# Kernel tuning notes

Hardware: AMD Instinct MI355X
Metric: run time of the kernel (lower is better)

## Reference

```python
import jax, jax.numpy as jnp
import numpy as np

N_NODES = 50000
N_EDGES = 800000
IN_DIM = 128
HID = 64
HEADS = 2
OUT_DIM = 2
N_GRAPHS = 512
NEG_SLOPE = 0.2


def setup_inputs() -> dict:
    key = jax.random.key(0)
    ks = jax.random.split(key, 16)
    x = jax.random.normal(ks[0], (N_NODES, IN_DIM), dtype=jnp.float32)
    edge_index = jax.random.randint(ks[1], (2, N_EDGES), 0, N_NODES, dtype=jnp.int64)
    batch = jnp.sort(jax.random.randint(ks[2], (N_NODES,), 0, N_GRAPHS, dtype=jnp.int64))
    s = 0.1
    W1 = jax.random.normal(ks[3], (IN_DIM, HEADS * HID), dtype=jnp.float32) * s
    a_src1 = jax.random.normal(ks[4], (HEADS, HID), dtype=jnp.float32) * s
    a_dst1 = jax.random.normal(ks[5], (HEADS, HID), dtype=jnp.float32) * s
    b1 = jnp.zeros((HEADS * HID,), dtype=jnp.float32)
    W2 = jax.random.normal(ks[6], (HEADS * HID, HID), dtype=jnp.float32) * s
    a_src2 = jax.random.normal(ks[7], (1, HID), dtype=jnp.float32) * s
    a_dst2 = jax.random.normal(ks[8], (1, HID), dtype=jnp.float32) * s
    b2 = jnp.zeros((HID,), dtype=jnp.float32)
    fcW = jax.random.normal(ks[9], (HID, OUT_DIM), dtype=jnp.float32) * s
    fcb = jnp.zeros((OUT_DIM,), dtype=jnp.float32)
    return dict(x=x, edge_index=edge_index, batch=batch,
                W1=W1, a_src1=a_src1, a_dst1=a_dst1, b1=b1,
                W2=W2, a_src2=a_src2, a_dst2=a_dst2, b2=b2,
                fcW=fcW, fcb=fcb)


def gat_layer(x, src, dst, W, a_src, a_dst, b, heads, c_out):
    # x: [N, F] -> h: [N, H, C]
    N = x.shape[0]
    h = (x @ W).reshape(N, heads, c_out)
    alpha_s = jnp.sum(h * a_src, axis=-1)  # [N, H]
    alpha_d = jnp.sum(h * a_dst, axis=-1)  # [N, H]
    e = jax.nn.leaky_relu(alpha_s[src] + alpha_d[dst], NEG_SLOPE)  # [E, H]
    # segment softmax over destination nodes
    emax = jax.ops.segment_max(e, dst, num_segments=N)  # [N, H]
    ex = jnp.exp(e - emax[dst])
    denom = jax.ops.segment_sum(ex, dst, num_segments=N)  # [N, H]
    coef = ex / denom[dst]  # [E, H]
    msg = h[src] * coef[..., None]  # [E, H, C]
    out = jax.ops.segment_sum(msg, dst, num_segments=N)  # [N, H, C]
    return out.reshape(N, heads * c_out) + b


def reference(x, edge_index, batch, W1, a_src1, a_dst1, b1, W2, a_src2, a_dst2, b2, fcW, fcb):
    N = x.shape[0]
    # PyG GATConv add_self_loops=True (shared graph for both layers)
    loops = jnp.arange(N, dtype=edge_index.dtype)
    src = jnp.concatenate([edge_index[0], loops])
    dst = jnp.concatenate([edge_index[1], loops])
    h = jax.nn.relu(gat_layer(x, src, dst, W1, a_src1, a_dst1, b1, HEADS, HID))
    h = jax.nn.relu(gat_layer(h, src, dst, W2, a_src2, a_dst2, b2, 1, HID))
    # global mean pool over graphs
    sums = jax.ops.segment_sum(h, batch, num_segments=N_GRAPHS)  # [G, HID]
    cnts = jax.ops.segment_sum(jnp.ones((N,), dtype=h.dtype), batch, num_segments=N_GRAPHS)
    pooled = sums / jnp.maximum(cnts, 1.0)[:, None]
    logits = pooled @ fcW + fcb
    return jax.nn.log_softmax(logits, axis=1)
```

## Files before the change

kernel.cpp:

```cpp
#include <hip/hip_runtime.h>
#include <math.h>

#define N_NODES 50000
#define N_EDGES 800000
#define EP (N_EDGES + N_NODES)
#define IN_DIM 128
#define HID 64
#define HEADS 2
#define OUT_DIM 2
#define N_GRAPHS 512
#define NEG_SLOPE 0.2f
#define NB_SCAN 196

typedef unsigned int uint;
typedef unsigned short ushort;

__device__ __forceinline__ ushort f2bf(float f) {
    uint u = __float_as_uint(f);
    u += 0x7fffu + ((u >> 16) & 1u);
    return (ushort)(u >> 16);
}
__device__ __forceinline__ float bf_lo(uint u) { return __uint_as_float(u << 16); }
__device__ __forceinline__ float bf_hi(uint u) { return __uint_as_float(u & 0xffff0000u); }

__global__ void hist_kernel(const int* __restrict__ ei, int* __restrict__ cnt,
                            int* __restrict__ erank) {
    int i = blockIdx.x * blockDim.x + threadIdx.x;
    if (i >= EP) return;
    int d = (i < N_EDGES) ? ei[N_EDGES + i] : (i - N_EDGES);
    erank[i] = atomicAdd(&cnt[d], 1);
}

__global__ void partial_kernel(const int* __restrict__ cnt, int* __restrict__ bsum) {
    int tid = threadIdx.x;
    int i = blockIdx.x * 256 + tid;
    int lane = tid & 63, wid = tid >> 6;
    int v = (i < N_NODES) ? cnt[i] : 0;
#pragma unroll
    for (int off = 32; off; off >>= 1) v += __shfl_xor(v, off);
    __shared__ int wsum[4];
    if (lane == 0) wsum[wid] = v;
    __syncthreads();
    if (tid == 0) bsum[blockIdx.x] = wsum[0] + wsum[1] + wsum[2] + wsum[3];
}

__global__ void scanb_kernel(const int* __restrict__ bsum, int* __restrict__ boff,
                             int* __restrict__ rowptr) {
    int tid = threadIdx.x;
    int lane = tid & 63, wid = tid >> 6;
    int v = (tid < NB_SCAN) ? bsum[tid] : 0;
    int incl = v;
#pragma unroll
    for (int off = 1; off < 64; off <<= 1) {
        int t = __shfl_up(incl, off);
        if (lane >= off) incl += t;
    }
    __shared__ int wt[4];
    if (lane == 63) wt[wid] = incl;
    __syncthreads();
    int add = 0;
    for (int w = 0; w < wid; w++) add += wt[w];
    incl += add;
    if (tid < NB_SCAN) boff[tid] = incl - v;
    if (tid == NB_SCAN - 1) rowptr[N_NODES] = incl;
}

__global__ void scanc_kernel(const int* __restrict__ cnt, const int* __restrict__ boff,
                             int* __restrict__ rowptr) {
    int tid = threadIdx.x;
    int i = blockIdx.x * 256 + tid;
    int lane = tid & 63, wid = tid >> 6;
    int v = (i < N_NODES) ? cnt[i] : 0;
    int incl = v;
#pragma unroll
    for (int off = 1; off < 64; off <<= 1) {
        int t = __shfl_up(incl, off);
        if (lane >= off) incl += t;
    }
    __shared__ int wt[4];
    if (lane == 63) wt[wid] = incl;
    __syncthreads();
    int add = boff[blockIdx.x];
    for (int w = 0; w < wid; w++) add += wt[w];
    int excl = add + incl - v;
    if (i < N_NODES) rowptr[i] = excl;
}

__global__ void scatter_kernel(const int* __restrict__ ei, const int* __restrict__ rowptr,
                               const int* __restrict__ erank, int* __restrict__ csr_src) {
    int i = blockIdx.x * blockDim.x + threadIdx.x;
    if (i >= EP) return;
    int s, d;
    if (i < N_EDGES) { s = ei[i]; d = ei[N_EDGES + i]; }
    else             { s = d = i - N_EDGES; }
    csr_src[rowptr[d] + erank[i]] = s;
}

__global__ void gemm_alphas1(const float* __restrict__ X, const float* __restrict__ W,
                             ushort* __restrict__ Y,
                             const float* __restrict__ a_src, const float* __restrict__ a_dst,
                             float* __restrict__ as, float* __restrict__ ad, int n_nodes) {
    __shared__ float xs[8][128];
    const int base = blockIdx.x * 8;
    const int t = threadIdx.x;
    const float4* X4 = (const float4*)X;
    for (int idx = t; idx < 8 * 32; idx += 64) {
        int r = idx >> 5, c = idx & 31;
        int n = base + r;
        float4 v = (n < n_nodes) ? X4[(size_t)n * 32 + c] : make_float4(0.f, 0.f, 0.f, 0.f);
        ((float4*)xs[r])[c] = v;
    }
    __syncthreads();

    float acc0[8], acc1[8];
#pragma unroll
    for (int i = 0; i < 8; i++) { acc0[i] = 0.f; acc1[i] = 0.f; }
    for (int k = 0; k < 128; k += 4) {
        float wA[4], wB[4];
#pragma unroll
        for (int kk = 0; kk < 4; kk++) {
            wA[kk] = W[(size_t)(k + kk) * 128 + t];
            wB[kk] = W[(size_t)(k + kk) * 128 + 64 + t];
        }
#pragma unroll
        for (int i = 0; i < 8; i++) {
            float4 xv = *(const float4*)&xs[i][k];
            float xx0 = xv.x, xx1 = xv.y, xx2 = xv.z, xx3 = xv.w;
            acc0[i] = fmaf(xx0, wA[0], acc0[i]); acc1[i] = fmaf(xx0, wB[0], acc1[i]);
            acc0[i] = fmaf(xx1, wA[1], acc0[i]); acc1[i] = fmaf(xx1, wB[1], acc1[i]);
            acc0[i] = fmaf(xx2, wA[2], acc0[i]); acc1[i] = fmaf(xx2, wB[2], acc1[i]);
            acc0[i] = fmaf(xx3, wA[3], acc0[i]); acc1[i] = fmaf(xx3, wB[3], acc1[i]);
        }
    }

    const float asv0 = a_src[t],      adv0 = a_dst[t];
    const float asv1 = a_src[64 + t], adv1 = a_dst[64 + t];
#pragma unroll
    for (int i = 0; i < 8; i++) {
        int n = base + i;
        if (n >= n_nodes) continue;
        Y[(size_t)n * 128 + t]      = f2bf(acc0[i]);
        Y[(size_t)n * 128 + 64 + t] = f2bf(acc1[i]);
        float s0 = acc0[i] * asv0, d0 = acc0[i] * adv0;
        float s1 = acc1[i] * asv1, d1 = acc1[i] * adv1;
#pragma unroll
        for (int off = 32; off; off >>= 1) {
            s0 += __shfl_xor(s0, off);
            d0 += __shfl_xor(d0, off);
            s1 += __shfl_xor(s1, off);
            d1 += __shfl_xor(d1, off);
        }
        if (t == 0) {
            as[(size_t)n * 2 + 0] = s0; as[(size_t)n * 2 + 1] = s1;
            ad[(size_t)n * 2 + 0] = d0; ad[(size_t)n * 2 + 1] = d1;
        }
    }
}

__global__ void gemm_alphas2(const float* __restrict__ X, const float* __restrict__ W,
                             ushort* __restrict__ Y,
                             const float* __restrict__ a_src, const float* __restrict__ a_dst,
                             float* __restrict__ as, float* __restrict__ ad, int n_nodes) {
    __shared__ float xs[8][128];
    const int base = blockIdx.x * 8;
    const int t = threadIdx.x;
    const int g = t >> 5, c = t & 31;
    const float4* X4 = (const float4*)X;
    for (int idx = t; idx < 8 * 32; idx += 64) {
        int r = idx >> 5, cc = idx & 31;
        int n = base + r;
        float4 v = (n < n_nodes) ? X4[(size_t)n * 32 + cc] : make_float4(0.f, 0.f, 0.f, 0.f);
        ((float4*)xs[r])[cc] = v;
    }
    __syncthreads();

    float acc0[4], acc1[4];
#pragma unroll
    for (int i = 0; i < 4; i++) { acc0[i] = 0.f; acc1[i] = 0.f; }
    for (int k = 0; k < 128; k += 4) {
        float wA[4], wB[4];
#pragma unroll
        for (int kk = 0; kk < 4; kk++) {
            wA[kk] = W[(size_t)(k + kk) * 64 + c];
            wB[kk] = W[(size_t)(k + kk) * 64 + 32 + c];
        }
#pragma unroll
        for (int i = 0; i < 4; i++) {
            float4 xv = *(const float4*)&xs[g * 4 + i][k];
            float xx0 = xv.x, xx1 = xv.y, xx2 = xv.z, xx3 = xv.w;
            acc0[i] = fmaf(xx0, wA[0], acc0[i]); acc1[i] = fmaf(xx0, wB[0], acc1[i]);
            acc0[i] = fmaf(xx1, wA[1], acc0[i]); acc1[i] = fmaf(xx1, wB[1], acc1[i]);
            acc0[i] = fmaf(xx2, wA[2], acc0[i]); acc1[i] = fmaf(xx2, wB[2], acc1[i]);
            acc0[i] = fmaf(xx3, wA[3], acc0[i]); acc1[i] = fmaf(xx3, wB[3], acc1[i]);
        }
    }

    const float asvA = a_src[c], asvB = a_src[32 + c];
    const float advA = a_dst[c], advB = a_dst[32 + c];
#pragma unroll
    for (int i = 0; i < 4; i++) {
        int n = base + g * 4 + i;
        if (n >= n_nodes) continue;
        Y[(size_t)n * 64 + c]      = f2bf(acc0[i]);
        Y[(size_t)n * 64 + 32 + c] = f2bf(acc1[i]);
        float s = acc0[i] * asvA + acc1[i] * asvB;
        float d = acc0[i] * advA + acc1[i] * advB;
#pragma unroll
        for (int off = 16; off; off >>= 1) {
            s += __shfl_xor(s, off);
            d += __shfl_xor(d, off);
        }
        if (c == 0) { as[n] = s; ad[n] = d; }
    }
}

__device__ __forceinline__ float lrelu(float e) { return e > 0.f ? e : NEG_SLOPE * e; }

__global__ void node_agg1_kernel(const int* __restrict__ rowptr, const int* __restrict__ csr_src,
                                 const uint* __restrict__ Hb,
                                 const float* __restrict__ as, const float* __restrict__ ad,
                                 const float* __restrict__ b, float* __restrict__ outp) {
    int wave = threadIdx.x >> 6;
    int lane = threadIdx.x & 63;
    int node = blockIdx.x * 4 + wave;
    if (node >= N_NODES) return;
    const int lo = rowptr[node], hi = rowptr[node + 1];
    const float ad0 = ad[(size_t)node * 2 + 0], ad1 = ad[(size_t)node * 2 + 1];

    float exa0 = 0.f, exa1 = 0.f, exb0 = 0.f, exb1 = 0.f;
    int j1 = lo + lane;
    if (j1 < hi) {
        int s = csr_src[j1];
        float2 a = *(const float2*)&as[(size_t)s * 2];
        exa0 = __expf(lrelu(a.x + ad0));
        exa1 = __expf(lrelu(a.y + ad1));
    }
    int j2 = lo + 64 + lane;
    if (j2 < hi) {
        int s = csr_src[j2];
        float2 a = *(const float2*)&as[(size_t)s * 2];
        exb0 = __expf(lrelu(a.x + ad0));
        exb1 = __expf(lrelu(a.y + ad1));
    }
    float d0 = exa0 + exb0, d1 = exa1 + exb1;
    for (int j = lo + 128 + lane; j < hi; j += 64) {
        int s = csr_src[j];
        float2 a = *(const float2*)&as[(size_t)s * 2];
        d0 += __expf(lrelu(a.x + ad0));
        d1 += __expf(lrelu(a.y + ad1));
    }
#pragma unroll
    for (int off = 32; off; off >>= 1) {
        d0 += __shfl_xor(d0, off);
        d1 += __shfl_xor(d1, off);
    }
    const float inv = (lane < 32) ? (1.f / d0) : (1.f / d1);
    const bool h0side = (lane < 32);

    float acc0 = 0.f, acc1 = 0.f;
    const int deg = hi - lo;
    const int n1 = deg < 64 ? deg : 64;
    int j = 0;
    for (; j + 4 <= n1; j += 4) {
        int s0 = csr_src[lo + j + 0], s1 = csr_src[lo + j + 1];
        int s2 = csr_src[lo + j + 2], s3 = csr_src[lo + j + 3];
        float ca0 = __shfl(exa0, j + 0), cb0 = __shfl(exa1, j + 0);
        float ca1 = __shfl(exa0, j + 1), cb1 = __shfl(exa1, j + 1);
        float ca2 = __shfl(exa0, j + 2), cb2 = __shfl(exa1, j + 2);
        float ca3 = __shfl(exa0, j + 3), cb3 = __shfl(exa1, j + 3);
        float c0 = h0side ? ca0 : cb0;
        float c1 = h0side ? ca1 : cb1;
        float c2 = h0side ? ca2 : cb2;
        float c3 = h0side ? ca3 : cb3;
        uint u0 = Hb[(size_t)s0 * 64 + lane];
        uint u1 = Hb[(size_t)s1 * 64 + lane];
        uint u2 = Hb[(size_t)s2 * 64 + lane];
        uint u3 = Hb[(size_t)s3 * 64 + lane];
        acc0 = fmaf(bf_lo(u0), c0, acc0); acc1 = fmaf(bf_hi(u0), c0, acc1);
        acc0 = fmaf(bf_lo(u1), c1, acc0); acc1 = fmaf(bf_hi(u1), c1, acc1);
        acc0 = fmaf(bf_lo(u2), c2, acc0); acc1 = fmaf(bf_hi(u2), c2, acc1);
        acc0 = fmaf(bf_lo(u3), c3, acc0); acc1 = fmaf(bf_hi(u3), c3, acc1);
    }
    for (; j < n1; j++) {
        int s = csr_src[lo + j];
        float ca = __shfl(exa0, j), cb = __shfl(exa1, j);
        float c = h0side ? ca : cb;
        uint u = Hb[(size_t)s * 64 + lane];
        acc0 = fmaf(bf_lo(u), c, acc0);
        acc1 = fmaf(bf_hi(u), c, acc1);
    }
    if (deg > 64) {
        const int n2 = deg < 128 ? deg : 128;
        for (j = 64; j < n2; j++) {
            int s = csr_src[lo + j];
            float ca = __shfl(exb0, j - 64), cb = __shfl(exb1, j - 64);
            float c = h0side ? ca : cb;
            uint u = Hb[(size_t)s * 64 + lane];
            acc0 = fmaf(bf_lo(u), c, acc0);
            acc1 = fmaf(bf_hi(u), c, acc1);
        }
        for (int jj = lo + 128; jj < hi; jj++) {
            int s = csr_src[jj];
            float2 a = *(const float2*)&as[(size_t)s * 2];
            float e0 = __expf(lrelu(a.x + ad0));
            float e1 = __expf(lrelu(a.y + ad1));
            float c = h0side ? e0 : e1;
            uint u = Hb[(size_t)s * 64 + lane];
            acc0 = fmaf(bf_lo(u), c, acc0);
            acc1 = fmaf(bf_hi(u), c, acc1);
        }
    }
    float v0 = acc0 * inv + b[2 * lane];
    float v1 = acc1 * inv + b[2 * lane + 1];
    v0 = v0 > 0.f ? v0 : 0.f;
    v1 = v1 > 0.f ? v1 : 0.f;
    *(float2*)&outp[(size_t)node * 128 + 2 * lane] = make_float2(v0, v1);
}

__global__ void node_agg2_kernel(const int* __restrict__ rowptr, const int* __restrict__ csr_src,
                                 const ushort* __restrict__ Hb,
                                 const float* __restrict__ as, const float* __restrict__ ad,
                                 const float* __restrict__ b, float* __restrict__ outp) {
    int wave = threadIdx.x >> 6;
    int lane = threadIdx.x & 63;
    int node = blockIdx.x * 4 + wave;
    if (node >= N_NODES) return;
    const int lo = rowptr[node], hi = rowptr[node + 1];
    const float adN = ad[node];

    float exa = 0.f, exb = 0.f;
    int j1 = lo + lane;
    if (j1 < hi) exa = __expf(lrelu(as[csr_src[j1]] + adN));
    int j2 = lo + 64 + lane;
    if (j2 < hi) exb = __expf(lrelu(as[csr_src[j2]] + adN));
    float d = exa + exb;
    for (int j = lo + 128 + lane; j < hi; j += 64)
        d += __expf(lrelu(as[csr_src[j]] + adN));
#pragma unroll
    for (int off = 32; off; off >>= 1) d += __shfl_xor(d, off);
    const float inv = 1.f / d;

    float acc = 0.f;
    const int deg = hi - lo;
    const int n1 = deg < 64 ? deg : 64;
    int j = 0;
    for (; j + 4 <= n1; j += 4) {
        int s0 = csr_src[lo + j + 0], s1 = csr_src[lo + j + 1];
        int s2 = csr_src[lo + j + 2], s3 = csr_src[lo + j + 3];
        float c0 = __shfl(exa, j + 0), c1 = __shfl(exa, j + 1);
        float c2 = __shfl(exa, j + 2), c3 = __shfl(exa, j + 3);
        float h0 = __uint_as_float(((uint)Hb[(size_t)s0 * 64 + lane]) << 16);
        float h1 = __uint_as_float(((uint)Hb[(size_t)s1 * 64 + lane]) << 16);
        float h2 = __uint_as_float(((uint)Hb[(size_t)s2 * 64 + lane]) << 16);
        float h3 = __uint_as_float(((uint)Hb[(size_t)s3 * 64 + lane]) << 16);
        acc = fmaf(h0, c0, acc);
        acc = fmaf(h1, c1, acc);
        acc = fmaf(h2, c2, acc);
        acc = fmaf(h3, c3, acc);
    }
    for (; j < n1; j++) {
        float c = __shfl(exa, j);
        acc = fmaf(__uint_as_float(((uint)Hb[(size_t)csr_src[lo + j] * 64 + lane]) << 16), c, acc);
    }
    if (deg > 64) {
        const int n2 = deg < 128 ? deg : 128;
        for (j = 64; j < n2; j++) {
            float c = __shfl(exb, j - 64);
            acc = fmaf(__uint_as_float(((uint)Hb[(size_t)csr_src[lo + j] * 64 + lane]) << 16), c, acc);
        }
        for (int jj = lo + 128; jj < hi; jj++) {
            int s = csr_src[jj];
            float c = __expf(lrelu(as[s] + adN));
            acc = fmaf(__uint_as_float(((uint)Hb[(size_t)s * 64 + lane]) << 16), c, acc);
        }
    }
    float v = acc * inv + b[lane];
    outp[(size_t)node * 64 + lane] = v > 0.f ? v : 0.f;
}

__global__ void pool_fc_kernel(const float* __restrict__ act2,
                               const int* __restrict__ batch,
                               const float* __restrict__ fcW,
                               const float* __restrict__ fcb,
                               float* __restrict__ out) {
    int g = blockIdx.x;
    int tid = threadIdx.x;
    int wid = tid >> 6, c = tid & 63;
    __shared__ int slo, shi;
    if (tid == 0) {
        int lo = 0, hi = N_NODES;
        while (lo < hi) { int m = (lo + hi) >> 1; if (batch[m] < g) lo = m + 1; else hi = m; }
        slo = lo;
        lo = 0; hi = N_NODES;
        while (lo < hi) { int m = (lo + hi) >> 1; if (batch[m] < g + 1) lo = m + 1; else hi = m; }
        shi = lo;
    }
    __syncthreads();
    const int lo = slo, hi = shi;
    float sum = 0.f;
    for (int n = lo + wid; n < hi; n += 4) sum += act2[(size_t)n * HID + c];
    __shared__ float ps[4][HID];
    ps[wid][c] = sum;
    __syncthreads();
    if (wid == 0) {
        float t = ps[0][c] + ps[1][c] + ps[2][c] + ps[3][c];
        float cnt = (float)(hi - lo);
        __shared__ float pooled[HID];
        pooled[c] = t / fmaxf(cnt, 1.f);
        __syncthreads();
        __shared__ float ls[OUT_DIM];
        if (c < OUT_DIM) {
            float l = fcb[c];
#pragma unroll 8
            for (int k = 0; k < HID; k++) l = fmaf(pooled[k], fcW[k * OUT_DIM + c], l);
            ls[c] = l;
        }
        __syncthreads();
        if (c < OUT_DIM) {
            float m = fmaxf(ls[0], ls[1]);
            float lse = m + logf(expf(ls[0] - m) + expf(ls[1] - m));
            out[(size_t)g * OUT_DIM + c] = ls[c] - lse;
        }
    }
}

extern "C" void kernel_launch(void* const* d_in, const int* in_sizes, int n_in,
                              void* d_out, int out_size, void* d_ws, size_t ws_size,
                              hipStream_t stream) {
    const float* x    = (const float*)d_in[0];
    const int*   ei   = (const int*)d_in[1];
    const int*   batch= (const int*)d_in[2];
    const float* W1   = (const float*)d_in[3];
    const float* as1w = (const float*)d_in[4];
    const float* ad1w = (const float*)d_in[5];
    const float* b1   = (const float*)d_in[6];
    const float* W2   = (const float*)d_in[7];
    const float* as2w = (const float*)d_in[8];
    const float* ad2w = (const float*)d_in[9];
    const float* b2   = (const float*)d_in[10];
    const float* fcW  = (const float*)d_in[11];
    const float* fcb  = (const float*)d_in[12];

    const size_t N = N_NODES;
    float* ws = (float*)d_ws;
    ushort* h1b  = (ushort*)ws;
    float* act1  = ws + N * 64;
    ushort* h2b  = (ushort*)(act1 + N * 128);
    float* out2  = act1 + N * 128 + N * 32;
    float* alps1 = out2 + N * 64;
    float* alpd1 = alps1 + N * 2;
    float* alps2 = alpd1 + N * 2;
    float* alpd2 = alps2 + N;
    int* cnt     = (int*)(alpd2 + N);
    int* rowptr  = cnt + N;
    int* bsum    = rowptr + N + 1;
    int* boff    = bsum + NB_SCAN;
    int* erank   = boff + NB_SCAN;
    int* csr_src = erank + EP;

    hipMemsetAsync(cnt, 0, N * sizeof(int), stream);
    hist_kernel<<<(EP + 255) / 256, 256, 0, stream>>>(ei, cnt, erank);
    partial_kernel<<<NB_SCAN, 256, 0, stream>>>(cnt, bsum);
    scanb_kernel<<<1, 256, 0, stream>>>(bsum, boff, rowptr);
    scanc_kernel<<<NB_SCAN, 256, 0, stream>>>(cnt, boff, rowptr);
    scatter_kernel<<<(EP + 255) / 256, 256, 0, stream>>>(ei, rowptr, erank, csr_src);

    gemm_alphas1<<<(N + 7) / 8, 64, 0, stream>>>(
        x, W1, h1b, as1w, ad1w, alps1, alpd1, (int)N);
    node_agg1_kernel<<<(N + 3) / 4, 256, 0, stream>>>(
        rowptr, csr_src, (const uint*)h1b, alps1, alpd1, b1, act1);

    gemm_alphas2<<<(N + 7) / 8, 64, 0, stream>>>(
        act1, W2, h2b, as2w, ad2w, alps2, alpd2, (int)N);
    node_agg2_kernel<<<(N + 3) / 4, 256, 0, stream>>>(
        rowptr, csr_src, h2b, alps2, alpd2, b2, out2);

    pool_fc_kernel<<<N_GRAPHS, 256, 0, stream>>>(out2, batch, fcW, fcb, (float*)d_out);
}
```

Before: 310.5 us.

## Fuse layer-1 GEMM with edge histogram and widen aggregation unroll to 8

Merges the layer-1 projection GEMM and the destination-degree histogram into one launch. Blocks are partitioned by index: the first group does the GEMM with 4 waves per block, each wave owning 8 nodes, and the rest do the atomic histogram. This lets the independent compute-bound and atomic-bound work overlap and removes one launch. Both aggregation kernels also unroll the neighbor loop from 4 to 8 and issue all gathers before the shuffles, for more memory-level parallelism at the cost of extra registers.

```diff
diff --git a/kernel.cpp b/kernel.cpp
--- a/kernel.cpp
+++ b/kernel.cpp
@@ -11,6 +11,8 @@
 #define N_GRAPHS 512
 #define NEG_SLOPE 0.2f
 #define NB_SCAN 196
+#define G_GEMM1 1563
+#define G_HIST 3321
 
 typedef unsigned int uint;
 typedef unsigned short ushort;
@@ -23,12 +25,75 @@
 __device__ __forceinline__ float bf_lo(uint u) { return __uint_as_float(u << 16); }
 __device__ __forceinline__ float bf_hi(uint u) { return __uint_as_float(u & 0xffff0000u); }
 
-__global__ void hist_kernel(const int* __restrict__ ei, int* __restrict__ cnt,
-                            int* __restrict__ erank) {
-    int i = blockIdx.x * blockDim.x + threadIdx.x;
-    if (i >= EP) return;
-    int d = (i < N_EDGES) ? ei[N_EDGES + i] : (i - N_EDGES);
-    erank[i] = atomicAdd(&cnt[d], 1);
+__global__ void fused_gemm1_hist(const float* __restrict__ X, const float* __restrict__ W,
+                                 ushort* __restrict__ Y,
+                                 const float* __restrict__ a_src, const float* __restrict__ a_dst,
+                                 float* __restrict__ as, float* __restrict__ ad,
+                                 const int* __restrict__ ei, int* __restrict__ cnt,
+                                 int* __restrict__ erank) {
+    if (blockIdx.x >= G_GEMM1) {
+        int i = (blockIdx.x - G_GEMM1) * 256 + threadIdx.x;
+        if (i < EP) {
+            int d = (i < N_EDGES) ? ei[N_EDGES + i] : (i - N_EDGES);
+            erank[i] = atomicAdd(&cnt[d], 1);
+        }
+        return;
+    }
+    __shared__ float xs[32][128];
+    const int wave = threadIdx.x >> 6;
+    const int lane = threadIdx.x & 63;
+    const int base = blockIdx.x * 32 + wave * 8;
+    const float4* X4 = (const float4*)X;
+    for (int idx = lane; idx < 8 * 32; idx += 64) {
+        int r = idx >> 5, c = idx & 31;
+        int n = base + r;
+        float4 v = (n < N_NODES) ? X4[(size_t)n * 32 + c] : make_float4(0.f, 0.f, 0.f, 0.f);
+        ((float4*)xs[wave * 8 + r])[c] = v;
+    }
+    __syncthreads();
+
+    float acc0[8], acc1[8];
+#pragma unroll
+    for (int i = 0; i < 8; i++) { acc0[i] = 0.f; acc1[i] = 0.f; }
+    for (int k = 0; k < 128; k += 4) {
+        float wA[4], wB[4];
+#pragma unroll
+        for (int kk = 0; kk < 4; kk++) {
+            wA[kk] = W[(size_t)(k + kk) * 128 + lane];
+            wB[kk] = W[(size_t)(k + kk) * 128 + 64 + lane];
+        }
+#pragma unroll
+        for (int i = 0; i < 8; i++) {
+            float4 xv = *(const float4*)&xs[wave * 8 + i][k];
+            acc0[i] = fmaf(xv.x, wA[0], acc0[i]); acc1[i] = fmaf(xv.x, wB[0], acc1[i]);
+            acc0[i] = fmaf(xv.y, wA[1], acc0[i]); acc1[i] = fmaf(xv.y, wB[1], acc1[i]);
+            acc0[i] = fmaf(xv.z, wA[2], acc0[i]); acc1[i] = fmaf(xv.z, wB[2], acc1[i]);
+            acc0[i] = fmaf(xv.w, wA[3], acc0[i]); acc1[i] = fmaf(xv.w, wB[3], acc1[i]);
+        }
+    }
+
+    const float asv0 = a_src[lane],      adv0 = a_dst[lane];
+    const float asv1 = a_src[64 + lane], adv1 = a_dst[64 + lane];
+#pragma unroll
+    for (int i = 0; i < 8; i++) {
+        int n = base + i;
+        if (n >= N_NODES) continue;
+        Y[(size_t)n * 128 + lane]      = f2bf(acc0[i]);
+        Y[(size_t)n * 128 + 64 + lane] = f2bf(acc1[i]);
+        float s0 = acc0[i] * asv0, d0 = acc0[i] * adv0;
+        float s1 = acc1[i] * asv1, d1 = acc1[i] * adv1;
+#pragma unroll
+        for (int off = 32; off; off >>= 1) {
+            s0 += __shfl_xor(s0, off);
+            d0 += __shfl_xor(d0, off);
+            s1 += __shfl_xor(s1, off);
+            d1 += __shfl_xor(d1, off);
+        }
+        if (lane == 0) {
+            as[(size_t)n * 2 + 0] = s0; as[(size_t)n * 2 + 1] = s1;
+            ad[(size_t)n * 2 + 0] = d0; ad[(size_t)n * 2 + 1] = d1;
+        }
+    }
 }
 
 __global__ void partial_kernel(const int* __restrict__ cnt, int* __restrict__ bsum) {
@@ -94,67 +159,6 @@
     if (i < N_EDGES) { s = ei[i]; d = ei[N_EDGES + i]; }
     else             { s = d = i - N_EDGES; }
     csr_src[rowptr[d] + erank[i]] = s;
-}
-
-__global__ void gemm_alphas1(const float* __restrict__ X, const float* __restrict__ W,
-                             ushort* __restrict__ Y,
-                             const float* __restrict__ a_src, const float* __restrict__ a_dst,
-                             float* __restrict__ as, float* __restrict__ ad, int n_nodes) {
-    __shared__ float xs[8][128];
-    const int base = blockIdx.x * 8;
-    const int t = threadIdx.x;
-    const float4* X4 = (const float4*)X;
-    for (int idx = t; idx < 8 * 32; idx += 64) {
-        int r = idx >> 5, c = idx & 31;
-        int n = base + r;
-        float4 v = (n < n_nodes) ? X4[(size_t)n * 32 + c] : make_float4(0.f, 0.f, 0.f, 0.f);
-        ((float4*)xs[r])[c] = v;
-    }
-    __syncthreads();
-
-    float acc0[8], acc1[8];
-#pragma unroll
-    for (int i = 0; i < 8; i++) { acc0[i] = 0.f; acc1[i] = 0.f; }
-    for (int k = 0; k < 128; k += 4) {
-        float wA[4], wB[4];
-#pragma unroll
-        for (int kk = 0; kk < 4; kk++) {
-            wA[kk] = W[(size_t)(k + kk) * 128 + t];
-            wB[kk] = W[(size_t)(k + kk) * 128 + 64 + t];
-        }
-#pragma unroll
-        for (int i = 0; i < 8; i++) {
-            float4 xv = *(const float4*)&xs[i][k];
-            float xx0 = xv.x, xx1 = xv.y, xx2 = xv.z, xx3 = xv.w;
-            acc0[i] = fmaf(xx0, wA[0], acc0[i]); acc1[i] = fmaf(xx0, wB[0], acc1[i]);
-            acc0[i] = fmaf(xx1, wA[1], acc0[i]); acc1[i] = fmaf(xx1, wB[1], acc1[i]);
-            acc0[i] = fmaf(xx2, wA[2], acc0[i]); acc1[i] = fmaf(xx2, wB[2], acc1[i]);
-            acc0[i] = fmaf(xx3, wA[3], acc0[i]); acc1[i] = fmaf(xx3, wB[3], acc1[i]);
-        }
-    }
-
-    const float asv0 = a_src[t],      adv0 = a_dst[t];
-    const float asv1 = a_src[64 + t], adv1 = a_dst[64 + t];
-#pragma unroll
-    for (int i = 0; i < 8; i++) {
-        int n = base + i;
-        if (n >= n_nodes) continue;
-        Y[(size_t)n * 128 + t]      = f2bf(acc0[i]);
-        Y[(size_t)n * 128 + 64 + t] = f2bf(acc1[i]);
-        float s0 = acc0[i] * asv0, d0 = acc0[i] * adv0;
-        float s1 = acc1[i] * asv1, d1 = acc1[i] * adv1;
-#pragma unroll
-        for (int off = 32; off; off >>= 1) {
-            s0 += __shfl_xor(s0, off);
-            d0 += __shfl_xor(d0, off);
-            s1 += __shfl_xor(s1, off);
-            d1 += __shfl_xor(d1, off);
-        }
-        if (t == 0) {
-            as[(size_t)n * 2 + 0] = s0; as[(size_t)n * 2 + 1] = s1;
-            ad[(size_t)n * 2 + 0] = d0; ad[(size_t)n * 2 + 1] = d1;
-        }
-    }
 }
 
 __global__ void gemm_alphas2(const float* __restrict__ X, const float* __restrict__ W,
@@ -187,11 +191,10 @@
 #pragma unroll
         for (int i = 0; i < 4; i++) {
             float4 xv = *(const float4*)&xs[g * 4 + i][k];
-            float xx0 = xv.x, xx1 = xv.y, xx2 = xv.z, xx3 = xv.w;
-            acc0[i] = fmaf(xx0, wA[0], acc0[i]); acc1[i] = fmaf(xx0, wB[0], acc1[i]);
-            acc0[i] = fmaf(xx1, wA[1], acc0[i]); acc1[i] = fmaf(xx1, wB[1], acc1[i]);
-            acc0[i] = fmaf(xx2, wA[2], acc0[i]); acc1[i] = fmaf(xx2, wB[2], acc1[i]);
-            acc0[i] = fmaf(xx3, wA[3], acc0[i]); acc1[i] = fmaf(xx3, wB[3], acc1[i]);
+            acc0[i] = fmaf(xv.x, wA[0], acc0[i]); acc1[i] = fmaf(xv.x, wB[0], acc1[i]);
+            acc0[i] = fmaf(xv.y, wA[1], acc0[i]); acc1[i] = fmaf(xv.y, wB[1], acc1[i]);
+            acc0[i] = fmaf(xv.z, wA[2], acc0[i]); acc1[i] = fmaf(xv.z, wB[2], acc1[i]);
+            acc0[i] = fmaf(xv.w, wA[3], acc0[i]); acc1[i] = fmaf(xv.w, wB[3], acc1[i]);
         }
     }
 
@@ -261,25 +264,43 @@
     const int deg = hi - lo;
     const int n1 = deg < 64 ? deg : 64;
     int j = 0;
-    for (; j + 4 <= n1; j += 4) {
+    for (; j + 8 <= n1; j += 8) {
         int s0 = csr_src[lo + j + 0], s1 = csr_src[lo + j + 1];
         int s2 = csr_src[lo + j + 2], s3 = csr_src[lo + j + 3];
+        int s4 = csr_src[lo + j + 4], s5 = csr_src[lo + j + 5];
+        int s6 = csr_src[lo + j + 6], s7 = csr_src[lo + j + 7];
+        uint u0 = Hb[(size_t)s0 * 64 + lane];
+        uint u1 = Hb[(size_t)s1 * 64 + lane];
+        uint u2 = Hb[(size_t)s2 * 64 + lane];
+        uint u3 = Hb[(size_t)s3 * 64 + lane];
+        uint u4 = Hb[(size_t)s4 * 64 + lane];
+        uint u5 = Hb[(size_t)s5 * 64 + lane];
+        uint u6 = Hb[(size_t)s6 * 64 + lane];
+        uint u7 = Hb[(size_t)s7 * 64 + lane];
         float ca0 = __shfl(exa0, j + 0), cb0 = __shfl(exa1, j + 0);
         float ca1 = __shfl(exa0, j + 1), cb1 = __shfl(exa1, j + 1);
         float ca2 = __shfl(exa0, j + 2), cb2 = __shfl(exa1, j + 2);
         float ca3 = __shfl(exa0, j + 3), cb3 = __shfl(exa1, j + 3);
+        float ca4 = __shfl(exa0, j + 4), cb4 = __shfl(exa1, j + 4);
+        float ca5 = __shfl(exa0, j + 5), cb5 = __shfl(exa1, j + 5);
+        float ca6 = __shfl(exa0, j + 6), cb6 = __shfl(exa1, j + 6);
+        float ca7 = __shfl(exa0, j + 7), cb7 = __shfl(exa1, j + 7);
         float c0 = h0side ? ca0 : cb0;
         float c1 = h0side ? ca1 : cb1;
         float c2 = h0side ? ca2 : cb2;
         float c3 = h0side ? ca3 : cb3;
-        uint u0 = Hb[(size_t)s0 * 64 + lane];
-        uint u1 = Hb[(size_t)s1 * 64 + lane];
-        uint u2 = Hb[(size_t)s2 * 64 + lane];
-        uint u3 = Hb[(size_t)s3 * 64 + lane];
+        float c4 = h0side ? ca4 : cb4;
+        float c5 = h0side ? ca5 : cb5;
+        float c6 = h0side ? ca6 : cb6;
+        float c7 = h0side ? ca7 : cb7;
         acc0 = fmaf(bf_lo(u0), c0, acc0); acc1 = fmaf(bf_hi(u0), c0, acc1);
         acc0 = fmaf(bf_lo(u1), c1, acc0); acc1 = fmaf(bf_hi(u1), c1, acc1);
         acc0 = fmaf(bf_lo(u2), c2, acc0); acc1 = fmaf(bf_hi(u2), c2, acc1);
         acc0 = fmaf(bf_lo(u3), c3, acc0); acc1 = fmaf(bf_hi(u3), c3, acc1);
+        acc0 = fmaf(bf_lo(u4), c4, acc0); acc1 = fmaf(bf_hi(u4), c4, acc1);
+        acc0 = fmaf(bf_lo(u5), c5, acc0); acc1 = fmaf(bf_hi(u5), c5, acc1);
+        acc0 = fmaf(bf_lo(u6), c6, acc0); acc1 = fmaf(bf_hi(u6), c6, acc1);
+        acc0 = fmaf(bf_lo(u7), c7, acc0); acc1 = fmaf(bf_hi(u7), c7, acc1);
     }
     for (; j < n1; j++) {
         int s = csr_src[lo + j];
@@ -344,19 +365,31 @@
     const int deg = hi - lo;
     const int n1 = deg < 64 ? deg : 64;
     int j = 0;
-    for (; j + 4 <= n1; j += 4) {
+    for (; j + 8 <= n1; j += 8) {
         int s0 = csr_src[lo + j + 0], s1 = csr_src[lo + j + 1];
         int s2 = csr_src[lo + j + 2], s3 = csr_src[lo + j + 3];
-        float c0 = __shfl(exa, j + 0), c1 = __shfl(exa, j + 1);
-        float c2 = __shfl(exa, j + 2), c3 = __shfl(exa, j + 3);
+        int s4 = csr_src[lo + j + 4], s5 = csr_src[lo + j + 5];
+        int s6 = csr_src[lo + j + 6], s7 = csr_src[lo + j + 7];
         float h0 = __uint_as_float(((uint)Hb[(size_t)s0 * 64 + lane]) << 16);
         float h1 = __uint_as_float(((uint)Hb[(size_t)s1 * 64 + lane]) << 16);
         float h2 = __uint_as_float(((uint)Hb[(size_t)s2 * 64 + lane]) << 16);
         float h3 = __uint_as_float(((uint)Hb[(size_t)s3 * 64 + lane]) << 16);
+        float h4 = __uint_as_float(((uint)Hb[(size_t)s4 * 64 + lane]) << 16);
+        float h5 = __uint_as_float(((uint)Hb[(size_t)s5 * 64 + lane]) << 16);
+        float h6 = __uint_as_float(((uint)Hb[(size_t)s6 * 64 + lane]) << 16);
+        float h7 = __uint_as_float(((uint)Hb[(size_t)s7 * 64 + lane]) << 16);
+        float c0 = __shfl(exa, j + 0), c1 = __shfl(exa, j + 1);
+        float c2 = __shfl(exa, j + 2), c3 = __shfl(exa, j + 3);
+        float c4 = __shfl(exa, j + 4), c5 = __shfl(exa, j + 5);
+        float c6 = __shfl(exa, j + 6), c7 = __shfl(exa, j + 7);
         acc = fmaf(h0, c0, acc);
         acc = fmaf(h1, c1, acc);
         acc = fmaf(h2, c2, acc);
         acc = fmaf(h3, c3, acc);
+        acc = fmaf(h4, c4, acc);
+        acc = fmaf(h5, c5, acc);
+        acc = fmaf(h6, c6, acc);
+        acc = fmaf(h7, c7, acc);
     }
     for (; j < n1; j++) {
         float c = __shfl(exa, j);
@@ -459,14 +492,14 @@
     int* csr_src = erank + EP;
 
     hipMemsetAsync(cnt, 0, N * sizeof(int), stream);
-    hist_kernel<<<(EP + 255) / 256, 256, 0, stream>>>(ei, cnt, erank);
+    fused_gemm1_hist<<<G_GEMM1 + G_HIST, 256, 0, stream>>>(
+        x, W1, h1b, as1w, ad1w, alps1, alpd1, ei, cnt, erank);
+
     partial_kernel<<<NB_SCAN, 256, 0, stream>>>(cnt, bsum);
     scanb_kernel<<<1, 256, 0, stream>>>(bsum, boff, rowptr);
     scanc_kernel<<<NB_SCAN, 256, 0, stream>>>(cnt, boff, rowptr);
     scatter_kernel<<<(EP + 255) / 256, 256, 0, stream>>>(ei, rowptr, erank, csr_src);
 
-    gemm_alphas1<<<(N + 7) / 8, 64, 0, stream>>>(
-        x, W1, h1b, as1w, ad1w, alps1, alpd1, (int)N);
     node_agg1_kernel<<<(N + 3) / 4, 256, 0, stream>>>(
         rowptr, csr_src, (const uint*)h1b, alps1, alpd1, b1, act1);
 
```

After: 291.3 us. 1.07x faster.
